# Performance work log

Measured on AMD Instinct MI355X. Metric: run time of the kernel, lower is better.

Reference implementation:

```python
import jax, jax.numpy as jnp
import numpy as np

N, D_FEAT, T, H = 4000, 6, 60, 64


def _gru_layer(inp, Wih, Whh, bih, bhh):
    # inp: [N, T, in]; torch GRU gate math, gate order (r, z, n)
    x_proj = inp @ Wih.T + bih  # [N, T, 3H]
    h0 = jnp.zeros((inp.shape[0], Whh.shape[1]), inp.dtype)

    def step(h, xp):
        gh = h @ Whh.T + bhh
        xr, xz, xn = jnp.split(xp, 3, axis=-1)
        hr, hz, hn = jnp.split(gh, 3, axis=-1)
        r = jax.nn.sigmoid(xr + hr)
        z = jax.nn.sigmoid(xz + hz)
        n = jnp.tanh(xn + r * hn)
        h = (1.0 - z) * n + z * h
        return h, h

    _, hs = jax.lax.scan(step, h0, jnp.transpose(x_proj, (1, 0, 2)))  # [T, N, H]
    return jnp.transpose(hs, (1, 0, 2))  # [N, T, H]


def setup_inputs():
    key = jax.random.key(0)
    ks = jax.random.split(key, 16)
    s = 1.0 / np.sqrt(H)
    u = lambda k, shape: jax.random.uniform(k, shape, jnp.float32, -s, s)
    inp = {
        "x": jax.random.normal(ks[0], (N, D_FEAT * T), jnp.float32),
        "relation_matrix": jax.random.randint(ks[1], (N, N, 3), 0, 2).astype(jnp.float32),
        "W_ih0": u(ks[2], (3 * H, D_FEAT)),
        "W_hh0": u(ks[3], (3 * H, H)),
        "b_ih0": u(ks[4], (3 * H,)),
        "b_hh0": u(ks[5], (3 * H,)),
        "W_ih1": u(ks[6], (3 * H, H)),
        "W_hh1": u(ks[7], (3 * H, H)),
        "b_ih1": u(ks[8], (3 * H,)),
        "b_hh1": u(ks[9], (3 * H,)),
        "W": jax.random.normal(ks[10], (2 * H, 1), jnp.float32) * np.sqrt(6.0 / (2 * H + 1)),
        "b": jnp.zeros((), jnp.float32),
        "fc_w": u(ks[11], (1, 2 * H)),
        "fc_b": u(ks[12], (1,)),
    }
    return inp


def reference(x, relation_matrix, W_ih0, W_hh0, b_ih0, b_hh0,
              W_ih1, W_hh1, b_ih1, b_hh1, W, b, fc_w, fc_b):
    n = x.shape[0]
    # [N, d_feat*T] -> [N, T, d_feat]
    xh = jnp.transpose(x.reshape(n, D_FEAT, -1), (0, 2, 1))
    xh = _gru_layer(xh, W_ih0, W_hh0, b_ih0, b_hh0)
    xh = _gru_layer(xh, W_ih1, W_hh1, b_ih1, b_hh1)
    x_hidden = xh[:, -1, :]  # [N, H]

    # concat(ei, hidden_batch) @ W == a_i + c_j  (avoid O(N^2 * 2H) tensor)
    a = x_hidden @ W[:H, 0]   # [N]
    c = x_hidden @ W[H:, 0]   # [N]
    weight = jax.nn.leaky_relu(a[:, None] + c[None, :] + b, 0.01)  # [N, N]

    mask = relation_matrix.sum(axis=2)  # [N, N]
    valid_weight = jnp.where(mask == 0, -1000000.0, mask * weight)
    valid_weight = jax.nn.softmax(valid_weight, axis=1)

    hidden = valid_weight @ x_hidden            # [N, H]
    hidden = jnp.concatenate([x_hidden, hidden], axis=1)  # [N, 2H]
    pred = (hidden @ fc_w.T + fc_b).squeeze()   # [N]
    return pred
```

## Files before the change

### kernel.cpp

```cpp
#include <hip/hip_runtime.h>

#define NR 4000
#define TS 60
#define DF 6
#define HD 64
#define MB 16
#define ARB 32

typedef __attribute__((ext_vector_type(8))) short bf8_t;
typedef __attribute__((ext_vector_type(4))) short bf4_t;
typedef __attribute__((ext_vector_type(4))) float f32x4;

__device__ __forceinline__ float sigf(float x) { return 1.0f / (1.0f + __expf(-x)); }
__device__ __forceinline__ float tanhfast(float x) { return 1.0f - 2.0f / (1.0f + __expf(2.0f * x)); }

__device__ __forceinline__ unsigned short f2bf(float v) {
  union { float f; unsigned u; } x; x.f = v;
  unsigned r = (x.u + 0x7fffu + ((x.u >> 16) & 1u)) >> 16;
  return (unsigned short)r;
}
__device__ __forceinline__ float bf2f(unsigned short h) {
  union { unsigned u; float f; } y; y.u = ((unsigned)h) << 16; return y.f;
}
__device__ __forceinline__ void split8(const float* v, bf8_t& hi, bf8_t& lo) {
#pragma unroll
  for (int j = 0; j < 8; ++j) {
    unsigned short h = f2bf(v[j]);
    float rem = v[j] - bf2f(h);
    hi[j] = (short)h;
    lo[j] = (short)f2bf(rem);
  }
}

__global__ __launch_bounds__(256, 1) void gru_mfma(
    const float* __restrict__ x,
    const float* __restrict__ Wih0, const float* __restrict__ Whh0,
    const float* __restrict__ bih0, const float* __restrict__ bhh0,
    const float* __restrict__ Wih1, const float* __restrict__ Whh1,
    const float* __restrict__ bih1, const float* __restrict__ bhh1,
    const float* __restrict__ Wac,
    float* __restrict__ xh_out, float* __restrict__ a_out, float* __restrict__ c_out) {
  __shared__ float xldsT[TS][MB][12];
  __shared__ unsigned short h0hiL[2][16][76];
  __shared__ unsigned short h0loL[2][16][76];
  __shared__ unsigned short h1hiL[2][16][76];
  __shared__ unsigned short h1loL[2][16][76];
  __shared__ float red[2][4][MB];

  const int tid = threadIdx.x;
  const int w = tid >> 6;
  const int lane = tid & 63;
  const int lg = lane >> 4;
  const int lm = lane & 15;
  const int unit = w * 16 + lm;
  const int r0 = blockIdx.x * MB;

  for (int idx = tid; idx < MB * 360; idx += 256) {
    int rr = idx / 360, cc = idx - rr * 360;
    int f = cc / 60, t = cc - f * 60;
    xldsT[t][rr][f] = x[(size_t)r0 * 360 + idx];
  }

  bf8_t wB[3][3][2][2];
  {
    const float* mats[3] = {Whh0, Wih1, Whh1};
#pragma unroll
    for (int m = 0; m < 3; ++m)
#pragma unroll
      for (int g = 0; g < 3; ++g)
#pragma unroll
        for (int kt = 0; kt < 2; ++kt) {
          const float* src = mats[m] + (size_t)(g * 64 + unit) * 64 + kt * 32 + 8 * lg;
          float v[8];
          *(float4*)&v[0] = *(const float4*)&src[0];
          *(float4*)&v[4] = *(const float4*)&src[4];
          split8(v, wB[m][g][kt][0], wB[m][g][kt][1]);
        }
  }
  float wih0g[3][DF];
#pragma unroll
  for (int g = 0; g < 3; ++g)
#pragma unroll
    for (int f = 0; f < DF; ++f)
      wih0g[g][f] = Wih0[(size_t)(g * 64 + unit) * DF + f];

  const float bi0r = bih0[unit], bi0z = bih0[64 + unit], bi0n = bih0[128 + unit];
  const float bh0r = bhh0[unit], bh0z = bhh0[64 + unit], bh0n = bhh0[128 + unit];
  const float c1R = bih1[unit] + bhh1[unit];
  const float c1Z = bih1[64 + unit] + bhh1[64 + unit];
  const float b1xn = bih1[128 + unit], b1hn = bhh1[128 + unit];

  bf8_t a0[2][2], a1[2][2];
  bf8_t zf = {};
#pragma unroll
  for (int kt = 0; kt < 2; ++kt)
#pragma unroll
    for (int h = 0; h < 2; ++h) { a0[kt][h] = zf; a1[kt][h] = zf; }
  float h0c[4] = {0.f, 0.f, 0.f, 0.f};
  float h1c[4] = {0.f, 0.f, 0.f, 0.f};

  __syncthreads();

#define MF(acc, A, B) acc = __builtin_amdgcn_mfma_f32_16x16x32_bf16(A, B, acc, 0, 0, 0)
#define MF3(acc, Af, Bf) do { \
    MF(acc, Af[0], Bf[0]); MF(acc, Af[0], Bf[1]); MF(acc, Af[1], Bf[0]); } while (0)

  for (int p = 0; p <= TS; ++p) {
    const bool doL0 = (p < TS);
    const bool doL1 = (p >= 1);
    const int par = p & 1;
    f32x4 aR, aZ, aN;
    float xn0[4];
    if (doL0) {
#pragma unroll
      for (int i = 0; i < 4; ++i) {
        const int row = 4 * lg + i;
        const float* xb = &xldsT[p][row][0];
        float4 x4 = *(const float4*)xb;
        float2 x2 = *(const float2*)(xb + 4);
        float sr = bi0r, sz = bi0z, sn = bi0n;
        sr = fmaf(wih0g[0][0], x4.x, sr); sz = fmaf(wih0g[1][0], x4.x, sz); sn = fmaf(wih0g[2][0], x4.x, sn);
        sr = fmaf(wih0g[0][1], x4.y, sr); sz = fmaf(wih0g[1][1], x4.y, sz); sn = fmaf(wih0g[2][1], x4.y, sn);
        sr = fmaf(wih0g[0][2], x4.z, sr); sz = fmaf(wih0g[1][2], x4.z, sz); sn = fmaf(wih0g[2][2], x4.z, sn);
        sr = fmaf(wih0g[0][3], x4.w, sr); sz = fmaf(wih0g[1][3], x4.w, sz); sn = fmaf(wih0g[2][3], x4.w, sn);
        sr = fmaf(wih0g[0][4], x2.x, sr); sz = fmaf(wih0g[1][4], x2.x, sz); sn = fmaf(wih0g[2][4], x2.x, sn);
        sr = fmaf(wih0g[0][5], x2.y, sr); sz = fmaf(wih0g[1][5], x2.y, sz); sn = fmaf(wih0g[2][5], x2.y, sn);
        aR[i] = sr + bh0r;
        aZ[i] = sz + bh0z;
        aN[i] = bh0n;
        xn0[i] = sn;
      }
#pragma unroll
      for (int kt = 0; kt < 2; ++kt) {
        MF3(aR, a0[kt], wB[0][0][kt]);
        MF3(aZ, a0[kt], wB[0][1][kt]);
        MF3(aN, a0[kt], wB[0][2][kt]);
      }
    }
    f32x4 R1, Z1, XN, HN;
    if (doL1) {
#pragma unroll
      for (int i = 0; i < 4; ++i) { R1[i] = c1R; Z1[i] = c1Z; XN[i] = b1xn; HN[i] = b1hn; }
#pragma unroll
      for (int kt = 0; kt < 2; ++kt) {
        MF3(R1, a0[kt], wB[1][0][kt]);
        MF3(Z1, a0[kt], wB[1][1][kt]);
        MF3(XN, a0[kt], wB[1][2][kt]);
        MF3(R1, a1[kt], wB[2][0][kt]);
        MF3(Z1, a1[kt], wB[2][1][kt]);
        MF3(HN, a1[kt], wB[2][2][kt]);
      }
    }
    if (doL0) {
#pragma unroll
      for (int i = 0; i < 4; ++i) {
        float r = sigf(aR[i]);
        float z = sigf(aZ[i]);
        float n = tanhfast(xn0[i] + r * aN[i]);
        h0c[i] = n + z * (h0c[i] - n);
        const int row = 4 * lg + i;
        unsigned u = __float_as_uint(h0c[i]);
        h0hiL[par][row][unit] = (unsigned short)(u >> 16);
        float lo = h0c[i] - __uint_as_float(u & 0xffff0000u);
        h0loL[par][row][unit] = (unsigned short)(__float_as_uint(lo) >> 16);
      }
    }
    if (doL1) {
#pragma unroll
      for (int i = 0; i < 4; ++i) {
        float r = sigf(R1[i]);
        float z = sigf(Z1[i]);
        float n = tanhfast(XN[i] + r * HN[i]);
        h1c[i] = n + z * (h1c[i] - n);
      }
      if (p < TS) {
#pragma unroll
        for (int i = 0; i < 4; ++i) {
          const int row = 4 * lg + i;
          unsigned u = __float_as_uint(h1c[i]);
          h1hiL[par][row][unit] = (unsigned short)(u >> 16);
          float lo = h1c[i] - __uint_as_float(u & 0xffff0000u);
          h1loL[par][row][unit] = (unsigned short)(__float_as_uint(lo) >> 16);
        }
      }
    }
    __syncthreads();
    if (p < TS) {
#pragma unroll
      for (int kt = 0; kt < 2; ++kt) {
        const int cb = kt * 32 + 8 * lg;
        bf4_t u0 = *(const bf4_t*)&h0hiL[par][lm][cb];
        bf4_t u1 = *(const bf4_t*)&h0hiL[par][lm][cb + 4];
        a0[kt][0] = __builtin_shufflevector(u0, u1, 0, 1, 2, 3, 4, 5, 6, 7);
        bf4_t l0 = *(const bf4_t*)&h0loL[par][lm][cb];
        bf4_t l1 = *(const bf4_t*)&h0loL[par][lm][cb + 4];
        a0[kt][1] = __builtin_shufflevector(l0, l1, 0, 1, 2, 3, 4, 5, 6, 7);
      }
      if (p >= 1) {
#pragma unroll
        for (int kt = 0; kt < 2; ++kt) {
          const int cb = kt * 32 + 8 * lg;
          bf4_t u0 = *(const bf4_t*)&h1hiL[par][lm][cb];
          bf4_t u1 = *(const bf4_t*)&h1hiL[par][lm][cb + 4];
          a1[kt][0] = __builtin_shufflevector(u0, u1, 0, 1, 2, 3, 4, 5, 6, 7);
          bf4_t l0 = *(const bf4_t*)&h1loL[par][lm][cb];
          bf4_t l1 = *(const bf4_t*)&h1loL[par][lm][cb + 4];
          a1[kt][1] = __builtin_shufflevector(l0, l1, 0, 1, 2, 3, 4, 5, 6, 7);
        }
      }
    }
  }
#undef MF3
#undef MF

#pragma unroll
  for (int i = 0; i < 4; ++i)
    xh_out[(size_t)(r0 + 4 * lg + i) * HD + unit] = h1c[i];

  const float WaU = Wac[unit], WcU = Wac[64 + unit];
#pragma unroll
  for (int i = 0; i < 4; ++i) {
    float av = h1c[i] * WaU, cv = h1c[i] * WcU;
#pragma unroll
    for (int off = 1; off < 16; off <<= 1) {
      av += __shfl_xor(av, off, 64);
      cv += __shfl_xor(cv, off, 64);
    }
    if (lm == 0) {
      red[0][w][4 * lg + i] = av;
      red[1][w][4 * lg + i] = cv;
    }
  }
  __syncthreads();
  if (tid < MB) {
    a_out[r0 + tid] = red[0][0][tid] + red[0][1][tid] + red[0][2][tid] + red[0][3][tid];
    c_out[r0 + tid] = red[1][0][tid] + red[1][1][tid] + red[1][2][tid] + red[1][3][tid];
  }
}

__global__ __launch_bounds__(256) void attn_part(
    const float* __restrict__ rel,
    const float* __restrict__ xh,
    const float* __restrict__ aArr, const float* __restrict__ cArr,
    const float* __restrict__ bSc,
    float* __restrict__ part, int jsl, int lsp) {
  __shared__ float xhl[64][68];
  __shared__ float pbuf[ARB][64];
  __shared__ float cls[1024];

  const int tid = threadIdx.x;
  const int rg = tid >> 5;
  const int tk = tid & 31;
  const int bx = blockIdx.x;
  const int ib = bx >> lsp;
  const int js = bx & ((1 << lsp) - 1);
  const int jbeg = js * jsl;
  const int jend = (jbeg + jsl < NR) ? (jbeg + jsl) : NR;
  const int nch = (jend - jbeg + 63) >> 6;
  const float bb = bSc[0];

  int irow[4];
  float aib[4];
#pragma unroll
  for (int rr = 0; rr < 4; ++rr) {
    irow[rr] = ib * ARB + rg + 8 * rr;
    aib[rr] = aArr[irow[rr]] + bb;
  }

  for (int t = tid; t < jsl; t += 256)
    cls[t] = (jbeg + t < NR) ? cArr[jbeg + t] : 0.f;

  float pr[4][6];
#pragma unroll
  for (int rr = 0; rr < 4; ++rr) {
    const float* rp = rel + (size_t)irow[rr] * (3 * NR) + (size_t)(jbeg + 2 * tk) * 3;
#pragma unroll
    for (int e = 0; e < 6; ++e) pr[rr][e] = rp[e];
  }

  float m[4], s[4], acc0[4], acc1[4];
#pragma unroll
  for (int rr = 0; rr < 4; ++rr) { m[rr] = -3.0e38f; s[rr] = 0.f; acc0[rr] = 0.f; acc1[rr] = 0.f; }

  for (int c = 0; c < nch; ++c) {
    const int j0 = jbeg + c * 64;
    __syncthreads();
    {
      const int jj = tid >> 2, seg = tid & 3;
      const int j = j0 + jj;
      if (j < NR) {
        const float4* src = (const float4*)(xh + (size_t)j * 64 + seg * 16);
#pragma unroll
        for (int q = 0; q < 4; ++q) *(float4*)&xhl[jj][seg * 16 + 4 * q] = src[q];
      } else {
        float4 z = {0.f, 0.f, 0.f, 0.f};
#pragma unroll
        for (int q = 0; q < 4; ++q) *(float4*)&xhl[jj][seg * 16 + 4 * q] = z;
      }
    }

    const int jb = j0 + 2 * tk;
    const bool ok = (jb < jend);
    const int ci = c * 64 + 2 * tk;
    const float cl0 = cls[ci], cl1 = cls[ci + 1];

#pragma unroll
    for (int rr = 0; rr < 4; ++rr) {
      float msum0 = pr[rr][0] + pr[rr][1] + pr[rr][2];
      float msum1 = pr[rr][3] + pr[rr][4] + pr[rr][5];
      float w0 = aib[rr] + cl0, w1 = aib[rr] + cl1;
      w0 = (w0 > 0.f) ? w0 : 0.01f * w0;
      w1 = (w1 > 0.f) ? w1 : 0.01f * w1;
      float v0 = (!ok) ? -3.0e37f : ((msum0 == 0.f) ? -1.0e6f : msum0 * w0);
      float v1 = (!ok) ? -3.0e37f : ((msum1 == 0.f) ? -1.0e6f : msum1 * w1);

      float lm2 = fmaxf(v0, v1);
#pragma unroll
      for (int off = 16; off; off >>= 1) lm2 = fmaxf(lm2, __shfl_xor(lm2, off, 32));
      const float mn = fmaxf(m[rr], lm2);
      const float f = __expf(m[rr] - mn);
      const float p0 = __expf(v0 - mn);
      const float p1 = __expf(v1 - mn);
      float ls = p0 + p1;
#pragma unroll
      for (int off = 16; off; off >>= 1) ls += __shfl_xor(ls, off, 32);
      s[rr] = s[rr] * f + ls;
      acc0[rr] *= f;
      acc1[rr] *= f;
      m[rr] = mn;
      pbuf[rg + 8 * rr][2 * tk] = p0;
      pbuf[rg + 8 * rr][2 * tk + 1] = p1;
    }

    if (c + 1 < nch) {
      const int jn = j0 + 64 + 2 * tk;
      if (jn < jend) {
#pragma unroll
        for (int rr = 0; rr < 4; ++rr) {
          const float* rp = rel + (size_t)irow[rr] * (3 * NR) + (size_t)jn * 3;
#pragma unroll
          for (int e = 0; e < 6; ++e) pr[rr][e] = rp[e];
        }
      }
    }

    __syncthreads();

#pragma unroll 2
    for (int j4 = 0; j4 < 16; ++j4) {
      float4 pv0 = *(const float4*)&pbuf[rg][4 * j4];
      float4 pv1 = *(const float4*)&pbuf[rg + 8][4 * j4];
      float4 pv2 = *(const float4*)&pbuf[rg + 16][4 * j4];
      float4 pv3 = *(const float4*)&pbuf[rg + 24][4 * j4];
      float2 x0 = *(const float2*)&xhl[4 * j4 + 0][2 * tk];
      float2 x1 = *(const float2*)&xhl[4 * j4 + 1][2 * tk];
      float2 x2 = *(const float2*)&xhl[4 * j4 + 2][2 * tk];
      float2 x3 = *(const float2*)&xhl[4 * j4 + 3][2 * tk];
      acc0[0] = fmaf(pv0.x, x0.x, acc0[0]); acc1[0] = fmaf(pv0.x, x0.y, acc1[0]);
      acc0[0] = fmaf(pv0.y, x1.x, acc0[0]); acc1[0] = fmaf(pv0.y, x1.y, acc1[0]);
      acc0[0] = fmaf(pv0.z, x2.x, acc0[0]); acc1[0] = fmaf(pv0.z, x2.y, acc1[0]);
      acc0[0] = fmaf(pv0.w, x3.x, acc0[0]); acc1[0] = fmaf(pv0.w, x3.y, acc1[0]);
      acc0[1] = fmaf(pv1.x, x0.x, acc0[1]); acc1[1] = fmaf(pv1.x, x0.y, acc1[1]);
      acc0[1] = fmaf(pv1.y, x1.x, acc0[1]); acc1[1] = fmaf(pv1.y, x1.y, acc1[1]);
      acc0[1] = fmaf(pv1.z, x2.x, acc0[1]); acc1[1] = fmaf(pv1.z, x2.y, acc1[1]);
      acc0[1] = fmaf(pv1.w, x3.x, acc0[1]); acc1[1] = fmaf(pv1.w, x3.y, acc1[1]);
      acc0[2] = fmaf(pv2.x, x0.x, acc0[2]); acc1[2] = fmaf(pv2.x, x0.y, acc1[2]);
      acc0[2] = fmaf(pv2.y, x1.x, acc0[2]); acc1[2] = fmaf(pv2.y, x1.y, acc1[2]);
      acc0[2] = fmaf(pv2.z, x2.x, acc0[2]); acc1[2] = fmaf(pv2.z, x2.y, acc1[2]);
      acc0[2] = fmaf(pv2.w, x3.x, acc0[2]); acc1[2] = fmaf(pv2.w, x3.y, acc1[2]);
      acc0[3] = fmaf(pv3.x, x0.x, acc0[3]); acc1[3] = fmaf(pv3.x, x0.y, acc1[3]);
      acc0[3] = fmaf(pv3.y, x1.x, acc0[3]); acc1[3] = fmaf(pv3.y, x1.y, acc1[3]);
      acc0[3] = fmaf(pv3.z, x2.x, acc0[3]); acc1[3] = fmaf(pv3.z, x2.y, acc1[3]);
      acc0[3] = fmaf(pv3.w, x3.x, acc0[3]); acc1[3] = fmaf(pv3.w, x3.y, acc1[3]);
    }
  }

#pragma unroll
  for (int rr = 0; rr < 4; ++rr) {
    float* base = part + ((size_t)bx * ARB + rg + 8 * rr) * 66;
    if (tk == 0) { base[0] = m[rr]; base[1] = s[rr]; }
    base[2 + 2 * tk] = acc0[rr];
    base[3 + 2 * tk] = acc1[rr];
  }
}

__global__ __launch_bounds__(256) void attn_combine(
    const float* __restrict__ part,
    const float* __restrict__ xh,
    const float* __restrict__ fcw, const float* __restrict__ fcb,
    float* __restrict__ pred, int nsplit) {
  const int tid = threadIdx.x;
  const int r = blockIdx.x * 4 + (tid >> 6);
  const int lane = tid & 63;
  const int ib = r / ARB, il = r % ARB;

  float mstar = -3.0e38f;
  for (int k = 0; k < nsplit; ++k) {
    const float* b = part + ((size_t)(ib * nsplit + k) * ARB + il) * 66;
    mstar = fmaxf(mstar, b[0]);
  }
  float sstar = 0.f, onum = 0.f;
  for (int k = 0; k < nsplit; ++k) {
    const float* b = part + ((size_t)(ib * nsplit + k) * ARB + il) * 66;
    const float wk = __expf(b[0] - mstar);
    sstar = fmaf(wk, b[1], sstar);
    onum = fmaf(wk, b[2 + lane], onum);
  }
  const float o = onum / sstar;
  float p = fcw[lane] * xh[(size_t)r * HD + lane] + fcw[64 + lane] * o;
#pragma unroll
  for (int off = 32; off; off >>= 1) p += __shfl_xor(p, off, 64);
  if (lane == 0) pred[r] = p + fcb[0];
}

extern "C" void kernel_launch(void* const* d_in, const int* in_sizes, int n_in,
                              void* d_out, int out_size, void* d_ws, size_t ws_size,
                              hipStream_t stream) {
  const float* x    = (const float*)d_in[0];
  const float* rel  = (const float*)d_in[1];
  const float* Wih0 = (const float*)d_in[2];
  const float* Whh0 = (const float*)d_in[3];
  const float* bih0 = (const float*)d_in[4];
  const float* bhh0 = (const float*)d_in[5];
  const float* Wih1 = (const float*)d_in[6];
  const float* Whh1 = (const float*)d_in[7];
  const float* bih1 = (const float*)d_in[8];
  const float* bhh1 = (const float*)d_in[9];
  const float* Wac  = (const float*)d_in[10];
  const float* bSc  = (const float*)d_in[11];
  const float* fcw  = (const float*)d_in[12];
  const float* fcb  = (const float*)d_in[13];

  float* xh   = (float*)d_ws;
  float* aA   = xh + (size_t)NR * HD;
  float* cA   = aA + NR;
  float* part = cA + NR;
  float* pred = (float*)d_out;

  int nsplit = 8, lsp = 3;
  size_t needB = ((size_t)NR * HD + 2 * NR +
                  (size_t)(NR / ARB) * 8 * ARB * 66) * 4;
  if (ws_size < needB) { nsplit = 4; lsp = 2; }
  const int jsl = NR / nsplit;

  gru_mfma<<<NR / MB, 256, 0, stream>>>(x, Wih0, Whh0, bih0, bhh0, Wih1, Whh1,
                                        bih1, bhh1, Wac, xh, aA, cA);
  attn_part<<<(NR / ARB) * nsplit, 256, 0, stream>>>(rel, xh, aA, cA, bSc, part, jsl, lsp);
  attn_combine<<<NR / 4, 256, 0, stream>>>(part, xh, fcw, fcb, pred, nsplit);
}
```

Before: 180.7 us.

## Split GRU block across 8 waves by row halves; move low weight parts to LDS

The GRU kernel goes from 256 to 512 threads per block. Two wave groups each handle 8 of the 16 rows, so each lane now evaluates two gate elements per step instead of four, which halves the serial activation and state-update work per wave. To fit more waves per CU, the low-precision halves of the split bf16 weights move from registers into shared memory and are reloaded before each MFMA triple, while the high halves stay in registers. Each wave still issues the full 16-row MFMAs, so matrix-core work per step doubles. In return the kernel gets fewer registers, two blocks per CU, and extra LDS traffic on the recurrent critical path.

After: 216.0 us. 19.5% more time.

```diff
diff --git a/kernel.cpp b/kernel.cpp
--- a/kernel.cpp
+++ b/kernel.cpp
@@ -32,7 +32,7 @@
   }
 }
 
-__global__ __launch_bounds__(256, 1) void gru_mfma(
+__global__ __launch_bounds__(512, 2) void gru_mfma(
     const float* __restrict__ x,
     const float* __restrict__ Wih0, const float* __restrict__ Whh0,
     const float* __restrict__ bih0, const float* __restrict__ bhh0,
@@ -40,7 +40,8 @@
     const float* __restrict__ bih1, const float* __restrict__ bhh1,
     const float* __restrict__ Wac,
     float* __restrict__ xh_out, float* __restrict__ a_out, float* __restrict__ c_out) {
-  __shared__ float xldsT[TS][MB][12];
+  __shared__ float xldsT[TS][MB][8];
+  __shared__ __align__(16) unsigned short BlL[3][3][2][64][4][8];
   __shared__ unsigned short h0hiL[2][16][76];
   __shared__ unsigned short h0loL[2][16][76];
   __shared__ unsigned short h1hiL[2][16][76];
@@ -49,19 +50,25 @@
 
   const int tid = threadIdx.x;
   const int w = tid >> 6;
+  const int wq = w & 3;
+  const int rg = w >> 2;
   const int lane = tid & 63;
   const int lg = lane >> 4;
   const int lm = lane & 15;
-  const int unit = w * 16 + lm;
+  const int unit = wq * 16 + lm;
   const int r0 = blockIdx.x * MB;
-
-  for (int idx = tid; idx < MB * 360; idx += 256) {
+  const bool hiHalf = (lg & 2) != 0;
+  const int arow0 = 4 * (lg & 1) + (lg & 2);
+  const int growA = rg * 8 + arow0;
+  const int growB = growA + 1;
+
+  for (int idx = tid; idx < MB * 360; idx += 512) {
     int rr = idx / 360, cc = idx - rr * 360;
     int f = cc / 60, t = cc - f * 60;
     xldsT[t][rr][f] = x[(size_t)r0 * 360 + idx];
   }
 
-  bf8_t wB[3][3][2][2];
+  bf8_t wH[3][3][2];
   {
     const float* mats[3] = {Whh0, Wih1, Whh1};
 #pragma unroll
@@ -74,7 +81,10 @@
           float v[8];
           *(float4*)&v[0] = *(const float4*)&src[0];
           *(float4*)&v[4] = *(const float4*)&src[4];
-          split8(v, wB[m][g][kt][0], wB[m][g][kt][1]);
+          bf8_t hi, lo;
+          split8(v, hi, lo);
+          wH[m][g][kt] = hi;
+          if (rg == 0) *(bf8_t*)&BlL[m][g][kt][unit][lg][0] = lo;
         }
   }
   float wih0g[3][DF];
@@ -96,115 +106,140 @@
   for (int kt = 0; kt < 2; ++kt)
 #pragma unroll
     for (int h = 0; h < 2; ++h) { a0[kt][h] = zf; a1[kt][h] = zf; }
-  float h0c[4] = {0.f, 0.f, 0.f, 0.f};
-  float h1c[4] = {0.f, 0.f, 0.f, 0.f};
+  float h0cA = 0.f, h0cB = 0.f, h1cA = 0.f, h1cB = 0.f;
 
   __syncthreads();
 
 #define MF(acc, A, B) acc = __builtin_amdgcn_mfma_f32_16x16x32_bf16(A, B, acc, 0, 0, 0)
-#define MF3(acc, Af, Bf) do { \
-    MF(acc, Af[0], Bf[0]); MF(acc, Af[0], Bf[1]); MF(acc, Af[1], Bf[0]); } while (0)
+#define MF3(acc, Af, mm, gg, ktt) do { \
+    bf8_t bl_ = *(const bf8_t*)&BlL[mm][gg][ktt][unit][lg][0]; \
+    MF(acc, Af[0], wH[mm][gg][ktt]); \
+    MF(acc, Af[0], bl_); \
+    MF(acc, Af[1], wH[mm][gg][ktt]); } while (0)
 
   for (int p = 0; p <= TS; ++p) {
-    const bool doL0 = (p < TS);
-    const bool doL1 = (p >= 1);
     const int par = p & 1;
     f32x4 aR, aZ, aN;
-    float xn0[4];
-    if (doL0) {
+    float sn[4];
+    if (p < TS) {
 #pragma unroll
       for (int i = 0; i < 4; ++i) {
-        const int row = 4 * lg + i;
+        const int row = rg * 8 + 4 * (lg & 1) + i;
         const float* xb = &xldsT[p][row][0];
         float4 x4 = *(const float4*)xb;
         float2 x2 = *(const float2*)(xb + 4);
-        float sr = bi0r, sz = bi0z, sn = bi0n;
-        sr = fmaf(wih0g[0][0], x4.x, sr); sz = fmaf(wih0g[1][0], x4.x, sz); sn = fmaf(wih0g[2][0], x4.x, sn);
-        sr = fmaf(wih0g[0][1], x4.y, sr); sz = fmaf(wih0g[1][1], x4.y, sz); sn = fmaf(wih0g[2][1], x4.y, sn);
-        sr = fmaf(wih0g[0][2], x4.z, sr); sz = fmaf(wih0g[1][2], x4.z, sz); sn = fmaf(wih0g[2][2], x4.z, sn);
-        sr = fmaf(wih0g[0][3], x4.w, sr); sz = fmaf(wih0g[1][3], x4.w, sz); sn = fmaf(wih0g[2][3], x4.w, sn);
-        sr = fmaf(wih0g[0][4], x2.x, sr); sz = fmaf(wih0g[1][4], x2.x, sz); sn = fmaf(wih0g[2][4], x2.x, sn);
-        sr = fmaf(wih0g[0][5], x2.y, sr); sz = fmaf(wih0g[1][5], x2.y, sz); sn = fmaf(wih0g[2][5], x2.y, sn);
-        aR[i] = sr + bh0r;
-        aZ[i] = sz + bh0z;
-        aN[i] = bh0n;
-        xn0[i] = sn;
+        float sr = bi0r + bh0r, sz = bi0z + bh0z, s_n = bi0n;
+        sr = fmaf(wih0g[0][0], x4.x, sr); sz = fmaf(wih0g[1][0], x4.x, sz); s_n = fmaf(wih0g[2][0], x4.x, s_n);
+        sr = fmaf(wih0g[0][1], x4.y, sr); sz = fmaf(wih0g[1][1], x4.y, sz); s_n = fmaf(wih0g[2][1], x4.y, s_n);
+        sr = fmaf(wih0g[0][2], x4.z, sr); sz = fmaf(wih0g[1][2], x4.z, sz); s_n = fmaf(wih0g[2][2], x4.z, s_n);
+        sr = fmaf(wih0g[0][3], x4.w, sr); sz = fmaf(wih0g[1][3], x4.w, sz); s_n = fmaf(wih0g[2][3], x4.w, s_n);
+        sr = fmaf(wih0g[0][4], x2.x, sr); sz = fmaf(wih0g[1][4], x2.x, sz); s_n = fmaf(wih0g[2][4], x2.x, s_n);
+        sr = fmaf(wih0g[0][5], x2.y, sr); sz = fmaf(wih0g[1][5], x2.y, sz); s_n = fmaf(wih0g[2][5], x2.y, s_n);
+        aR[i] = sr; aZ[i] = sz; aN[i] = bh0n; sn[i] = s_n;
       }
 #pragma unroll
       for (int kt = 0; kt < 2; ++kt) {
-        MF3(aR, a0[kt], wB[0][0][kt]);
-        MF3(aZ, a0[kt], wB[0][1][kt]);
-        MF3(aN, a0[kt], wB[0][2][kt]);
+        MF3(aR, a0[kt], 0, 0, kt);
+        MF3(aZ, a0[kt], 0, 1, kt);
+        MF3(aN, a0[kt], 0, 2, kt);
       }
     }
     f32x4 R1, Z1, XN, HN;
-    if (doL1) {
+    if (p >= 1) {
 #pragma unroll
       for (int i = 0; i < 4; ++i) { R1[i] = c1R; Z1[i] = c1Z; XN[i] = b1xn; HN[i] = b1hn; }
 #pragma unroll
       for (int kt = 0; kt < 2; ++kt) {
-        MF3(R1, a0[kt], wB[1][0][kt]);
-        MF3(Z1, a0[kt], wB[1][1][kt]);
-        MF3(XN, a0[kt], wB[1][2][kt]);
-        MF3(R1, a1[kt], wB[2][0][kt]);
-        MF3(Z1, a1[kt], wB[2][1][kt]);
-        MF3(HN, a1[kt], wB[2][2][kt]);
-      }
-    }
-    if (doL0) {
-#pragma unroll
-      for (int i = 0; i < 4; ++i) {
-        float r = sigf(aR[i]);
-        float z = sigf(aZ[i]);
-        float n = tanhfast(xn0[i] + r * aN[i]);
-        h0c[i] = n + z * (h0c[i] - n);
-        const int row = 4 * lg + i;
-        unsigned u = __float_as_uint(h0c[i]);
-        h0hiL[par][row][unit] = (unsigned short)(u >> 16);
-        float lo = h0c[i] - __uint_as_float(u & 0xffff0000u);
-        h0loL[par][row][unit] = (unsigned short)(__float_as_uint(lo) >> 16);
-      }
-    }
-    if (doL1) {
-#pragma unroll
-      for (int i = 0; i < 4; ++i) {
-        float r = sigf(R1[i]);
-        float z = sigf(Z1[i]);
-        float n = tanhfast(XN[i] + r * HN[i]);
-        h1c[i] = n + z * (h1c[i] - n);
-      }
-      if (p < TS) {
-#pragma unroll
-        for (int i = 0; i < 4; ++i) {
-          const int row = 4 * lg + i;
-          unsigned u = __float_as_uint(h1c[i]);
-          h1hiL[par][row][unit] = (unsigned short)(u >> 16);
-          float lo = h1c[i] - __uint_as_float(u & 0xffff0000u);
-          h1loL[par][row][unit] = (unsigned short)(__float_as_uint(lo) >> 16);
+        MF3(R1, a0[kt], 1, 0, kt);
+        MF3(Z1, a0[kt], 1, 1, kt);
+        MF3(XN, a0[kt], 1, 2, kt);
+        MF3(R1, a1[kt], 2, 0, kt);
+        MF3(Z1, a1[kt], 2, 1, kt);
+        MF3(HN, a1[kt], 2, 2, kt);
+      }
+    }
+    if (p < TS) {
+      const float xnA = hiHalf ? sn[2] : sn[0];
+      const float xnB = hiHalf ? sn[3] : sn[1];
+      {
+        float vR = hiHalf ? aR[2] : aR[0];
+        float vZ = hiHalf ? aZ[2] : aZ[0];
+        float vN = hiHalf ? aN[2] : aN[0];
+        float rr_ = sigf(vR), zz_ = sigf(vZ);
+        float nn_ = tanhfast(xnA + rr_ * vN);
+        h0cA = nn_ + zz_ * (h0cA - nn_);
+        unsigned u = __float_as_uint(h0cA);
+        h0hiL[par][growA][unit] = (unsigned short)(u >> 16);
+        float lo = h0cA - __uint_as_float(u & 0xffff0000u);
+        h0loL[par][growA][unit] = (unsigned short)(__float_as_uint(lo) >> 16);
+      }
+      {
+        float vR = hiHalf ? aR[3] : aR[1];
+        float vZ = hiHalf ? aZ[3] : aZ[1];
+        float vN = hiHalf ? aN[3] : aN[1];
+        float rr_ = sigf(vR), zz_ = sigf(vZ);
+        float nn_ = tanhfast(xnB + rr_ * vN);
+        h0cB = nn_ + zz_ * (h0cB - nn_);
+        unsigned u = __float_as_uint(h0cB);
+        h0hiL[par][growB][unit] = (unsigned short)(u >> 16);
+        float lo = h0cB - __uint_as_float(u & 0xffff0000u);
+        h0loL[par][growB][unit] = (unsigned short)(__float_as_uint(lo) >> 16);
+      }
+    }
+    if (p >= 1) {
+      {
+        float vR = hiHalf ? R1[2] : R1[0];
+        float vZ = hiHalf ? Z1[2] : Z1[0];
+        float vXN = hiHalf ? XN[2] : XN[0];
+        float vHN = hiHalf ? HN[2] : HN[0];
+        float rr_ = sigf(vR), zz_ = sigf(vZ);
+        float nn_ = tanhfast(vXN + rr_ * vHN);
+        h1cA = nn_ + zz_ * (h1cA - nn_);
+        if (p < TS) {
+          unsigned u = __float_as_uint(h1cA);
+          h1hiL[par][growA][unit] = (unsigned short)(u >> 16);
+          float lo = h1cA - __uint_as_float(u & 0xffff0000u);
+          h1loL[par][growA][unit] = (unsigned short)(__float_as_uint(lo) >> 16);
+        }
+      }
+      {
+        float vR = hiHalf ? R1[3] : R1[1];
+        float vZ = hiHalf ? Z1[3] : Z1[1];
+        float vXN = hiHalf ? XN[3] : XN[1];
+        float vHN = hiHalf ? HN[3] : HN[1];
+        float rr_ = sigf(vR), zz_ = sigf(vZ);
+        float nn_ = tanhfast(vXN + rr_ * vHN);
+        h1cB = nn_ + zz_ * (h1cB - nn_);
+        if (p < TS) {
+          unsigned u = __float_as_uint(h1cB);
+          h1hiL[par][growB][unit] = (unsigned short)(u >> 16);
+          float lo = h1cB - __uint_as_float(u & 0xffff0000u);
+          h1loL[par][growB][unit] = (unsigned short)(__float_as_uint(lo) >> 16);
         }
       }
     }
     __syncthreads();
     if (p < TS) {
+      const int frow = rg * 8 + (lm & 7);
 #pragma unroll
       for (int kt = 0; kt < 2; ++kt) {
         const int cb = kt * 32 + 8 * lg;
-        bf4_t u0 = *(const bf4_t*)&h0hiL[par][lm][cb];
-        bf4_t u1 = *(const bf4_t*)&h0hiL[par][lm][cb + 4];
+        bf4_t u0 = *(const bf4_t*)&h0hiL[par][frow][cb];
+        bf4_t u1 = *(const bf4_t*)&h0hiL[par][frow][cb + 4];
         a0[kt][0] = __builtin_shufflevector(u0, u1, 0, 1, 2, 3, 4, 5, 6, 7);
-        bf4_t l0 = *(const bf4_t*)&h0loL[par][lm][cb];
-        bf4_t l1 = *(const bf4_t*)&h0loL[par][lm][cb + 4];
+        bf4_t l0 = *(const bf4_t*)&h0loL[par][frow][cb];
+        bf4_t l1 = *(const bf4_t*)&h0loL[par][frow][cb + 4];
         a0[kt][1] = __builtin_shufflevector(l0, l1, 0, 1, 2, 3, 4, 5, 6, 7);
       }
       if (p >= 1) {
 #pragma unroll
         for (int kt = 0; kt < 2; ++kt) {
           const int cb = kt * 32 + 8 * lg;
-          bf4_t u0 = *(const bf4_t*)&h1hiL[par][lm][cb];
-          bf4_t u1 = *(const bf4_t*)&h1hiL[par][lm][cb + 4];
+          bf4_t u0 = *(const bf4_t*)&h1hiL[par][frow][cb];
+          bf4_t u1 = *(const bf4_t*)&h1hiL[par][frow][cb + 4];
           a1[kt][0] = __builtin_shufflevector(u0, u1, 0, 1, 2, 3, 4, 5, 6, 7);
-          bf4_t l0 = *(const bf4_t*)&h1loL[par][lm][cb];
-          bf4_t l1 = *(const bf4_t*)&h1loL[par][lm][cb + 4];
+          bf4_t l0 = *(const bf4_t*)&h1loL[par][frow][cb];
+          bf4_t l1 = *(const bf4_t*)&h1loL[par][frow][cb + 4];
           a1[kt][1] = __builtin_shufflevector(l0, l1, 0, 1, 2, 3, 4, 5, 6, 7);
         }
       }
@@ -213,22 +248,25 @@
 #undef MF3
 #undef MF
 
-#pragma unroll
-  for (int i = 0; i < 4; ++i)
-    xh_out[(size_t)(r0 + 4 * lg + i) * HD + unit] = h1c[i];
+  xh_out[(size_t)(r0 + growA) * HD + unit] = h1cA;
+  xh_out[(size_t)(r0 + growB) * HD + unit] = h1cB;
 
   const float WaU = Wac[unit], WcU = Wac[64 + unit];
-#pragma unroll
-  for (int i = 0; i < 4; ++i) {
-    float av = h1c[i] * WaU, cv = h1c[i] * WcU;
+  {
+    float av = h1cA * WaU, cv = h1cA * WcU;
+    float av2 = h1cB * WaU, cv2 = h1cB * WcU;
 #pragma unroll
     for (int off = 1; off < 16; off <<= 1) {
-      av += __shfl_xor(av, off, 64);
-      cv += __shfl_xor(cv, off, 64);
+      av += __shfl_xor(av, off, 16);
+      cv += __shfl_xor(cv, off, 16);
+      av2 += __shfl_xor(av2, off, 16);
+      cv2 += __shfl_xor(cv2, off, 16);
     }
     if (lm == 0) {
-      red[0][w][4 * lg + i] = av;
-      red[1][w][4 * lg + i] = cv;
+      red[0][wq][growA] = av;
+      red[1][wq][growA] = cv;
+      red[0][wq][growB] = av2;
+      red[1][wq][growB] = cv2;
     }
   }
   __syncthreads();
@@ -443,7 +481,7 @@
   if (ws_size < needB) { nsplit = 4; lsp = 2; }
   const int jsl = NR / nsplit;
 
-  gru_mfma<<<NR / MB, 256, 0, stream>>>(x, Wih0, Whh0, bih0, bhh0, Wih1, Whh1,
+  gru_mfma<<<NR / MB, 512, 0, stream>>>(x, Wih0, Whh0, bih0, bhh0, Wih1, Whh1,
                                         bih1, bhh1, Wac, xh, aA, cA);
   attn_part<<<(NR / ARB) * nsplit, 256, 0, stream>>>(rel, xh, aA, cA, bSc, part, jsl, lsp);
   attn_combine<<<NR / 4, 256, 0, stream>>>(part, xh, fcw, fcb, pred, nsplit);
```
